# Performance work log

Hardware: AMD Instinct MI355X
Metric: run time of the kernel (lower is better)

Reference implementation:

```python
import jax, jax.numpy as jnp
import numpy as np

N, F, H = 22, 448, 64
LN_EPS = 1e-5


def _layernorm(h, g, b):
    mu = h.mean(axis=-1, keepdims=True)
    var = ((h - mu) ** 2).mean(axis=-1, keepdims=True)
    return (h - mu) / jnp.sqrt(var + LN_EPS) * g + b


def setup_inputs() -> dict:
    key = jax.random.key(0)
    ks = jax.random.split(key, 16)
    B = 128
    x = jax.random.normal(ks[0], (B, N, F), dtype=jnp.float32)
    s = lambda fan_in: 1.0 / np.sqrt(fan_in)
    # correlation-branch edge_weight_net: Linear(2F,64) -> ReLU -> Linear(64,1) -> Sigmoid
    cw1 = jax.random.uniform(ks[1], (2 * F, 64), jnp.float32, -s(2 * F), s(2 * F))
    cb1 = jax.random.uniform(ks[2], (64,), jnp.float32, -s(2 * F), s(2 * F))
    cw2 = jax.random.uniform(ks[3], (64, 1), jnp.float32, -s(64), s(64))
    cb2 = jax.random.uniform(ks[4], (1,), jnp.float32, -s(64), s(64))
    # semantic branch
    emb = jax.random.normal(ks[5], (N, H), dtype=jnp.float32) * 0.01
    D = 2 * H + 2 * F
    sw1 = jax.random.uniform(ks[6], (D, H), jnp.float32, -s(D), s(D))
    sb1 = jax.random.uniform(ks[7], (H,), jnp.float32, -s(D), s(D))
    ln_g = jnp.ones((H,), jnp.float32)
    ln_b = jnp.zeros((H,), jnp.float32)
    sw2 = jax.random.uniform(ks[8], (H, H // 2), jnp.float32, -s(H), s(H))
    sb2 = jax.random.uniform(ks[9], (H // 2,), jnp.float32, -s(H), s(H))
    sw3 = jax.random.uniform(ks[10], (H // 2, 1), jnp.float32, -s(H // 2), s(H // 2))
    sb3 = jax.random.uniform(ks[11], (1,), jnp.float32, -s(H // 2), s(H // 2))
    thr = jnp.asarray(0.3, jnp.float32)
    alpha_p = jnp.asarray(0.6, jnp.float32)
    return dict(x=x, cw1=cw1, cb1=cb1, cw2=cw2, cb2=cb2, emb=emb,
                sw1=sw1, sb1=sb1, ln_g=ln_g, ln_b=ln_b,
                sw2=sw2, sb2=sb2, sw3=sw3, sb3=sb3,
                thr=thr, alpha_p=alpha_p)


def reference(x, cw1, cb1, cw2, cb2, emb, sw1, sb1, ln_g, ln_b,
              sw2, sb2, sw3, sb3, thr, alpha_p):
    B, n, f = x.shape
    eye = jnp.eye(n, dtype=x.dtype)[None]

    # ---- Correlation graph ----
    xc = x - x.mean(axis=-1, keepdims=True)
    std = jnp.std(x, axis=-1, ddof=1, keepdims=True) + 1e-8  # torch std is unbiased
    xn = xc / std
    corr = jnp.abs(jnp.einsum('bif,bjf->bij', xn, xn) / f)
    # pairwise edge features (B,N,N,2F)
    xi = jnp.broadcast_to(x[:, :, None, :], (B, n, n, f))
    xj = jnp.broadcast_to(x[:, None, :, :], (B, n, n, f))
    ef = jnp.concatenate([xi, xj], axis=-1)
    h = jax.nn.relu(ef @ cw1 + cb1)
    w_corr = jax.nn.sigmoid((h @ cw2 + cb2)[..., 0])
    g_corr = corr * w_corr + eye

    # ---- Semantic graph ----
    ei = jnp.broadcast_to(emb[None, :, None, :], (B, n, n, H))
    ej = jnp.broadcast_to(emb[None, None, :, :], (B, n, n, H))
    sf = jnp.concatenate([ei, ej, xi, xj], axis=-1)  # (B,N,N,2H+2F)
    h1 = jax.nn.relu(_layernorm(sf @ sw1 + sb1, ln_g, ln_b))
    h2 = jax.nn.relu(h1 @ sw2 + sb2)
    w_sem = jax.nn.sigmoid((h2 @ sw3 + sb3)[..., 0])  # (B,N,N)
    # original loop fills only i<j and mirrors; diagonal stays 0
    upper = jnp.triu(w_sem, k=1)
    adj = upper + jnp.swapaxes(upper, 1, 2)
    t = jax.nn.sigmoid(thr)
    adj = jnp.where(adj > t, adj, jnp.zeros_like(adj))
    g_sem = adj + eye

    # ---- Learned fusion ----
    alpha = jax.nn.sigmoid(alpha_p)
    return alpha * g_corr + (1.0 - alpha) * g_sem
```

## Files before the change

### kernel.cpp

```cpp
#include <hip/hip_runtime.h>
#include <math.h>

namespace {
constexpr int kN = 22;
constexpr int kF = 448;
constexpr int kNP = 484;
constexpr int kXStr = 452;
constexpr int kSm1 = kN * kXStr + 2 * kN;
constexpr int kAStr = 36;
constexpr int kBStr = 68;
constexpr int kPStr = 68;
constexpr int kVStr = 68;

__device__ __forceinline__ void map_slot(int s, int& i, int& j) {
    if (s < 231) {
        int rem = s, i0 = 0;
        while (rem >= 21 - i0) { rem -= 21 - i0; ++i0; }
        i = i0; j = i0 + 1 + rem;
    } else {
        i = j = s - 231;
    }
}
}

__global__ __launch_bounds__(256) void hgc_k1(
    const float* __restrict__ x,
    const float* __restrict__ cw1, const float* __restrict__ cb1,
    const float* __restrict__ emb,
    const float* __restrict__ sw1, const float* __restrict__ sb1,
    float* __restrict__ C, float* __restrict__ g,
    int M, int Mtiles, int nGemm)
{
    __shared__ __align__(16) float sm[kSm1];
    const int tid = threadIdx.x;

    if ((int)blockIdx.x < nGemm) {
        float* As = sm;
        float* Bs = sm + 64 * kAStr;
        const int bm = blockIdx.x % Mtiles;
        const int bn = blockIdx.x / Mtiles;
        const int m0 = bm * 32;

        const float* Wsrc =
            (bn == 0) ? cw1 :
            (bn == 1) ? cw1 + 448 * 64 :
            (bn == 2) ? sw1 + 128 * 64 :
                        sw1 + 576 * 64;

        const int tm = tid & 15;
        const int tn = tid >> 4;
        float acc[2][4];
        #pragma unroll
        for (int i = 0; i < 2; ++i)
            #pragma unroll
            for (int j = 0; j < 4; ++j) acc[i][j] = 0.f;

        float4 rA[2], rB[4];

        auto preMain = [&](int k0) {
            #pragma unroll
            for (int p = 0; p < 2; ++p) {
                const int idx = tid + p * 256;
                const int row = idx >> 4, kq = idx & 15;
                int m = m0 + row; if (m >= M) m = M - 1;
                rA[p] = *(const float4*)&x[(size_t)m * kF + k0 + kq * 4];
            }
            #pragma unroll
            for (int p = 0; p < 4; ++p) {
                const int idx = tid + p * 256;
                const int k = idx >> 4, nq = idx & 15;
                rB[p] = *(const float4*)&Wsrc[(size_t)(k0 + k) * 64 + nq * 4];
            }
        };
        auto preEmb = [&]() {
            const float* W2 = sw1 + (bn == 2 ? 0 : 64) * 64;
            #pragma unroll
            for (int p = 0; p < 2; ++p) {
                const int idx = tid + p * 256;
                const int row = idx >> 4, kq = idx & 15;
                const int r = (m0 + row) % kN;
                rA[p] = *(const float4*)&emb[(size_t)r * 64 + kq * 4];
            }
            #pragma unroll
            for (int p = 0; p < 4; ++p) {
                const int idx = tid + p * 256;
                const int k = idx >> 4, nq = idx & 15;
                rB[p] = *(const float4*)&W2[(size_t)k * 64 + nq * 4];
            }
        };
        auto commit = [&]() {
            #pragma unroll
            for (int p = 0; p < 2; ++p) {
                const int idx = tid + p * 256;
                const int row = idx >> 4, kq = idx & 15;
                As[(kq * 4 + 0) * kAStr + row] = rA[p].x;
                As[(kq * 4 + 1) * kAStr + row] = rA[p].y;
                As[(kq * 4 + 2) * kAStr + row] = rA[p].z;
                As[(kq * 4 + 3) * kAStr + row] = rA[p].w;
            }
            #pragma unroll
            for (int p = 0; p < 4; ++p) {
                const int idx = tid + p * 256;
                const int k = idx >> 4, nq = idx & 15;
                *(float4*)&Bs[k * kBStr + nq * 4] = rB[p];
            }
        };
        auto compute = [&]() {
            #pragma unroll 8
            for (int k = 0; k < 64; ++k) {
                const float2 a2 = *(const float2*)&As[k * kAStr + tm * 2];
                const float4 b4 = *(const float4*)&Bs[k * kBStr + tn * 4];
                acc[0][0] = fmaf(a2.x, b4.x, acc[0][0]);
                acc[0][1] = fmaf(a2.x, b4.y, acc[0][1]);
                acc[0][2] = fmaf(a2.x, b4.z, acc[0][2]);
                acc[0][3] = fmaf(a2.x, b4.w, acc[0][3]);
                acc[1][0] = fmaf(a2.y, b4.x, acc[1][0]);
                acc[1][1] = fmaf(a2.y, b4.y, acc[1][1]);
                acc[1][2] = fmaf(a2.y, b4.z, acc[1][2]);
                acc[1][3] = fmaf(a2.y, b4.w, acc[1][3]);
            }
        };

        preMain(0);
        commit();
        __syncthreads();
        for (int c = 0; c < 7; ++c) {
            if (c < 6) preMain((c + 1) * 64);
            else if (bn >= 2) preEmb();
            compute();
            __syncthreads();
            if (c < 6 || bn >= 2) {
                commit();
                __syncthreads();
            }
        }
        if (bn >= 2) compute();

        float4 bias = {0, 0, 0, 0};
        if (bn == 0)      bias = *(const float4*)&cb1[tn * 4];
        else if (bn == 2) bias = *(const float4*)&sb1[tn * 4];
        #pragma unroll
        for (int i = 0; i < 2; ++i) {
            const int m = m0 + tm * 2 + i;
            if (m < M) {
                float4 o;
                o.x = acc[i][0] + bias.x; o.y = acc[i][1] + bias.y;
                o.z = acc[i][2] + bias.z; o.w = acc[i][3] + bias.w;
                *(float4*)&C[(size_t)m * 256 + bn * 64 + tn * 4] = o;
            }
        }
    } else {
        float* smu = sm + kN * kXStr;
        float* sis = smu + kN;
        const int cb = blockIdx.x - nGemm;
        const int b = cb >> 1;
        const int r0 = (cb & 1) * 11;

        const float4* xb4 = (const float4*)(x + (size_t)b * (kN * kF));
        for (int idx = tid; idx < kN * kF / 4; idx += 256) {
            const float4 v = xb4[idx];
            const int r = idx / 112;
            const int k = (idx - r * 112) * 4;
            float* d = sm + r * kXStr + k;
            d[0] = v.x; d[1] = v.y; d[2] = v.z; d[3] = v.w;
        }
        __syncthreads();

        {
            const int wid = tid >> 6, lane = tid & 63;
            for (int r = wid; r < kN; r += 4) {
                const float* row = sm + r * kXStr;
                float s = 0.f;
                #pragma unroll
                for (int c = 0; c < 7; ++c) s += row[c * 64 + lane];
                #pragma unroll
                for (int o = 32; o; o >>= 1) s += __shfl_xor(s, o, 64);
                const float mean = s * (1.f / 448.f);
                float ss = 0.f;
                #pragma unroll
                for (int c = 0; c < 7; ++c) { const float d = row[c * 64 + lane] - mean; ss = fmaf(d, d, ss); }
                #pragma unroll
                for (int o = 32; o; o >>= 1) ss += __shfl_xor(ss, o, 64);
                if (lane == 0) {
                    smu[r] = mean;
                    sis[r] = 1.f / (sqrtf(ss * (1.f / 447.f)) + 1e-8f);
                }
            }
        }
        __syncthreads();

        for (int p = tid; p < 11 * kN; p += 256) {
            const int pi = p / 22;
            const int i = r0 + pi, j = p - pi * 22;
            const float4* ri = (const float4*)(sm + i * kXStr);
            const float4* rj = (const float4*)(sm + j * kXStr);
            float dot = 0.f;
            for (int q = 0; q < 112; ++q) {
                const float4 a = ri[q], bq = rj[q];
                dot = fmaf(a.x, bq.x, dot); dot = fmaf(a.y, bq.y, dot);
                dot = fmaf(a.z, bq.z, dot); dot = fmaf(a.w, bq.w, dot);
            }
            const float c = (dot - 448.f * smu[i] * smu[j]) * sis[i] * sis[j] * (1.f / 448.f);
            g[(size_t)b * kNP + i * 22 + j] = fabsf(c);
        }
    }
}

__global__ __launch_bounds__(256) void hgc_k2(
    const float* __restrict__ C, const float* __restrict__ g,
    const float* __restrict__ cw2, const float* __restrict__ cb2,
    const float* __restrict__ sw2, const float* __restrict__ sb2,
    const float* __restrict__ sw3, const float* __restrict__ sb3,
    const float* __restrict__ ln_g, const float* __restrict__ ln_b,
    const float* __restrict__ thr, const float* __restrict__ alpha_p,
    float* __restrict__ out)
{
    __shared__ __align__(16) float sp[4 * kN * kPStr];
    __shared__ float sg[kNP];
    __shared__ __align__(16) float sw2s[2048];
    __shared__ float scw2[64], slng[64], slnb[64], ssw3[32], ssb2[32];
    __shared__ __align__(16) float vbuf[32 * kVStr];

    const int tid = threadIdx.x;
    const int b   = blockIdx.x >> 2;
    const int pb  = blockIdx.x & 3;

    #pragma unroll
    for (int a = 0; a < 4; ++a) {
        float* dst = sp + a * kN * kPStr;
        for (int idx = tid; idx < 352; idx += 256) {
            const int r = idx >> 4, kq = idx & 15;
            const float4 v = *(const float4*)&C[((size_t)(b * 22 + r)) * 256 + a * 64 + kq * 4];
            *(float4*)&dst[r * kPStr + kq * 4] = v;
        }
    }
    for (int idx = tid; idx < kNP; idx += 256) sg[idx] = g[(size_t)b * kNP + idx];
    {
        const float4* s4 = (const float4*)sw2;
        for (int idx = tid; idx < 512; idx += 256)
            *((float4*)(sw2s + idx * 4)) = s4[idx];
    }
    if (tid < 64)       { scw2[tid] = cw2[tid]; slng[tid] = ln_g[tid]; slnb[tid] = ln_b[tid]; }
    else if (tid < 96)  { ssw3[tid - 64] = sw3[tid - 64]; }
    else if (tid < 128) { ssb2[tid - 96] = sb2[tid - 96]; }
    __syncthreads();

    const int pl = tid >> 3;
    const int t  = tid & 7;
    const float* sa1 = sp;
    const float* sa2 = sp + kN * kPStr;
    const float* su1 = sp + 2 * kN * kPStr;
    const float* su2 = sp + 3 * kN * kPStr;

    for (int ch = 0; ch < 2; ++ch) {
        const int s_ = pb * 64 + ch * 32 + pl;
        const bool valid = s_ < 253;
        const int s = valid ? s_ : 252;
        int i, j; map_slot(s, i, j);

        float zc1 = 0.f, zc2 = 0.f;
        {
            const float* a1i = sa1 + i * kPStr + t * 8;
            const float* a2j = sa2 + j * kPStr + t * 8;
            const float* a1j = sa1 + j * kPStr + t * 8;
            const float* a2i = sa2 + i * kPStr + t * 8;
            const float4 i0 = *(const float4*)a1i, i1 = *(const float4*)(a1i + 4);
            const float4 j0 = *(const float4*)a2j, j1 = *(const float4*)(a2j + 4);
            const float4 k0 = *(const float4*)a1j, k1 = *(const float4*)(a1j + 4);
            const float4 l0 = *(const float4*)a2i, l1 = *(const float4*)(a2i + 4);
            const float4 w0 = *(const float4*)(scw2 + t * 8);
            const float4 w1 = *(const float4*)(scw2 + t * 8 + 4);
            zc1 = fmaf(fmaxf(i0.x + j0.x, 0.f), w0.x, zc1);
            zc1 = fmaf(fmaxf(i0.y + j0.y, 0.f), w0.y, zc1);
            zc1 = fmaf(fmaxf(i0.z + j0.z, 0.f), w0.z, zc1);
            zc1 = fmaf(fmaxf(i0.w + j0.w, 0.f), w0.w, zc1);
            zc1 = fmaf(fmaxf(i1.x + j1.x, 0.f), w1.x, zc1);
            zc1 = fmaf(fmaxf(i1.y + j1.y, 0.f), w1.y, zc1);
            zc1 = fmaf(fmaxf(i1.z + j1.z, 0.f), w1.z, zc1);
            zc1 = fmaf(fmaxf(i1.w + j1.w, 0.f), w1.w, zc1);
            zc2 = fmaf(fmaxf(k0.x + l0.x, 0.f), w0.x, zc2);
            zc2 = fmaf(fmaxf(k0.y + l0.y, 0.f), w0.y, zc2);
            zc2 = fmaf(fmaxf(k0.z + l0.z, 0.f), w0.z, zc2);
            zc2 = fmaf(fmaxf(k0.w + l0.w, 0.f), w0.w, zc2);
            zc2 = fmaf(fmaxf(k1.x + l1.x, 0.f), w1.x, zc2);
            zc2 = fmaf(fmaxf(k1.y + l1.y, 0.f), w1.y, zc2);
            zc2 = fmaf(fmaxf(k1.z + l1.z, 0.f), w1.z, zc2);
            zc2 = fmaf(fmaxf(k1.w + l1.w, 0.f), w1.w, zc2);
            zc1 += __shfl_xor(zc1, 1, 64); zc1 += __shfl_xor(zc1, 2, 64); zc1 += __shfl_xor(zc1, 4, 64);
            zc2 += __shfl_xor(zc2, 1, 64); zc2 += __shfl_xor(zc2, 2, 64); zc2 += __shfl_xor(zc2, 4, 64);
        }

        float raw[8];
        float s1 = 0.f;
        {
            const float* pu1 = su1 + i * kPStr + t * 8;
            const float* pu2 = su2 + j * kPStr + t * 8;
            const float4 u0 = *(const float4*)pu1, u1v = *(const float4*)(pu1 + 4);
            const float4 v0 = *(const float4*)pu2, v1v = *(const float4*)(pu2 + 4);
            raw[0] = u0.x + v0.x; raw[1] = u0.y + v0.y; raw[2] = u0.z + v0.z; raw[3] = u0.w + v0.w;
            raw[4] = u1v.x + v1v.x; raw[5] = u1v.y + v1v.y; raw[6] = u1v.z + v1v.z; raw[7] = u1v.w + v1v.w;
            #pragma unroll
            for (int c = 0; c < 8; ++c) s1 += raw[c];
        }
        s1 += __shfl_xor(s1, 1, 64); s1 += __shfl_xor(s1, 2, 64); s1 += __shfl_xor(s1, 4, 64);
        const float mean = s1 * (1.f / 64.f);
        float s2 = 0.f;
        #pragma unroll
        for (int c = 0; c < 8; ++c) { const float d = raw[c] - mean; s2 = fmaf(d, d, s2); }
        s2 += __shfl_xor(s2, 1, 64); s2 += __shfl_xor(s2, 2, 64); s2 += __shfl_xor(s2, 4, 64);
        const float rstd = rsqrtf(s2 * (1.f / 64.f) + 1e-5f);
        {
            float* vb = vbuf + pl * kVStr + t * 8;
            float4 o0, o1;
            o0.x = fmaxf(fmaf((raw[0] - mean) * rstd, slng[t*8+0], slnb[t*8+0]), 0.f);
            o0.y = fmaxf(fmaf((raw[1] - mean) * rstd, slng[t*8+1], slnb[t*8+1]), 0.f);
            o0.z = fmaxf(fmaf((raw[2] - mean) * rstd, slng[t*8+2], slnb[t*8+2]), 0.f);
            o0.w = fmaxf(fmaf((raw[3] - mean) * rstd, slng[t*8+3], slnb[t*8+3]), 0.f);
            o1.x = fmaxf(fmaf((raw[4] - mean) * rstd, slng[t*8+4], slnb[t*8+4]), 0.f);
            o1.y = fmaxf(fmaf((raw[5] - mean) * rstd, slng[t*8+5], slnb[t*8+5]), 0.f);
            o1.z = fmaxf(fmaf((raw[6] - mean) * rstd, slng[t*8+6], slnb[t*8+6]), 0.f);
            o1.w = fmaxf(fmaf((raw[7] - mean) * rstd, slng[t*8+7], slnb[t*8+7]), 0.f);
            *(float4*)vb = o0;
            *(float4*)(vb + 4) = o1;
        }
        __syncthreads();

        float4 acc = {0, 0, 0, 0};
        {
            const float* vb = vbuf + pl * kVStr;
            for (int k = 0; k < 64; ++k) {
                const float v = vb[k];
                const float4 w = *((const float4*)(sw2s + k * 32 + t * 4));
                acc.x = fmaf(v, w.x, acc.x); acc.y = fmaf(v, w.y, acc.y);
                acc.z = fmaf(v, w.z, acc.z); acc.w = fmaf(v, w.w, acc.w);
            }
        }
        float z2;
        {
            const int o0 = t * 4;
            z2  = fmaxf(acc.x + ssb2[o0 + 0], 0.f) * ssw3[o0 + 0];
            z2 += fmaxf(acc.y + ssb2[o0 + 1], 0.f) * ssw3[o0 + 1];
            z2 += fmaxf(acc.z + ssb2[o0 + 2], 0.f) * ssw3[o0 + 2];
            z2 += fmaxf(acc.w + ssb2[o0 + 3], 0.f) * ssw3[o0 + 3];
            z2 += __shfl_xor(z2, 1, 64); z2 += __shfl_xor(z2, 2, 64); z2 += __shfl_xor(z2, 4, 64);
        }

        if (valid && t == 0) {
            const float alpha = 1.f / (1.f + __expf(-alpha_p[0]));
            const float wc1 = 1.f / (1.f + __expf(-(zc1 + cb2[0])));
            float gsem;
            if (i == j) {
                gsem = 1.f;
            } else {
                const float wsem = 1.f / (1.f + expf(-(z2 + sb3[0])));
                const float tt   = 1.f / (1.f + expf(-thr[0]));
                gsem = (wsem > tt) ? wsem : 0.f;
            }
            const float gc1 = fmaf(sg[i * 22 + j], wc1, (i == j) ? 1.f : 0.f);
            out[(size_t)b * kNP + i * 22 + j] = fmaf(alpha, gc1, (1.f - alpha) * gsem);
            if (i != j) {
                const float wc2 = 1.f / (1.f + __expf(-(zc2 + cb2[0])));
                const float gc2 = sg[j * 22 + i] * wc2;
                out[(size_t)b * kNP + j * 22 + i] = fmaf(alpha, gc2, (1.f - alpha) * gsem);
            }
        }
        __syncthreads();
    }
}

extern "C" void kernel_launch(void* const* d_in, const int* in_sizes, int n_in,
                              void* d_out, int out_size, void* d_ws, size_t ws_size,
                              hipStream_t stream)
{
    (void)n_in; (void)out_size; (void)ws_size;
    const float* x     = (const float*)d_in[0];
    const float* cw1   = (const float*)d_in[1];
    const float* cb1   = (const float*)d_in[2];
    const float* cw2   = (const float*)d_in[3];
    const float* cb2   = (const float*)d_in[4];
    const float* emb   = (const float*)d_in[5];
    const float* sw1   = (const float*)d_in[6];
    const float* sb1   = (const float*)d_in[7];
    const float* ln_g  = (const float*)d_in[8];
    const float* ln_b  = (const float*)d_in[9];
    const float* sw2   = (const float*)d_in[10];
    const float* sb2   = (const float*)d_in[11];
    const float* sw3   = (const float*)d_in[12];
    const float* sb3   = (const float*)d_in[13];
    const float* thr   = (const float*)d_in[14];
    const float* alpha = (const float*)d_in[15];
    float* out = (float*)d_out;
    float* ws  = (float*)d_ws;

    const int B = in_sizes[0] / (kN * kF);
    const int M = kN * B;
    const int Mtiles = (M + 31) / 32;
    const int nGemm = Mtiles * 4;

    float* C = ws;
    float* g = ws + (size_t)M * 256;

    hipLaunchKernelGGL(hgc_k1, dim3(nGemm + 2 * B), dim3(256), 0, stream,
                       x, cw1, cb1, emb, sw1, sb1, C, g, M, Mtiles, nGemm);
    hipLaunchKernelGGL(hgc_k2, dim3(4 * B), dim3(256), 0, stream,
                       C, g, cw2, cb2, sw2, sb2, sw3, sb3, ln_g, ln_b, thr, alpha, out);
}
```

Before: 126.8 us.

## Split-K GEMM tiles with 4x4 microtiles and single-pass transposed pair MLP

The projection GEMM in kernel 1 now splits the K dimension of each 64-wide chunk across two 128-thread halves. Each thread computes a 4x4 register microtile, and the two partial sums are combined through shared memory before bias and store. Kernel 2 now handles all 64 pair slots in one pass with 4 threads per slot instead of two 32-slot chunks, writing LayerNorm outputs transposed so the second-layer matvec can reuse each weight load across two slots. This cuts synchronisation rounds and LDS traffic per FMA, at the cost of an extra reduction step and more registers.

After: 128.9 us. About the same (+1.7%).

```diff
diff --git a/kernel.cpp b/kernel.cpp
--- a/kernel.cpp
+++ b/kernel.cpp
@@ -10,7 +10,7 @@
 constexpr int kAStr = 36;
 constexpr int kBStr = 68;
 constexpr int kPStr = 68;
-constexpr int kVStr = 68;
+constexpr int kTStr = 66;
 
 __device__ __forceinline__ void map_slot(int s, int& i, int& j) {
     if (s < 231) {
@@ -47,13 +47,13 @@
             (bn == 2) ? sw1 + 128 * 64 :
                         sw1 + 576 * 64;
 
-        const int tm = tid & 15;
-        const int tn = tid >> 4;
-        float acc[2][4];
+        const int kg   = tid >> 7;
+        const int t128 = tid & 127;
+        const int mg = t128 >> 4;
+        const int ng = t128 & 15;
+        float4 acc[4];
         #pragma unroll
-        for (int i = 0; i < 2; ++i)
-            #pragma unroll
-            for (int j = 0; j < 4; ++j) acc[i][j] = 0.f;
+        for (int i = 0; i < 4; ++i) acc[i] = float4{0, 0, 0, 0};
 
         float4 rA[2], rB[4];
 
@@ -107,17 +107,18 @@
         };
         auto compute = [&]() {
             #pragma unroll 8
-            for (int k = 0; k < 64; ++k) {
-                const float2 a2 = *(const float2*)&As[k * kAStr + tm * 2];
-                const float4 b4 = *(const float4*)&Bs[k * kBStr + tn * 4];
-                acc[0][0] = fmaf(a2.x, b4.x, acc[0][0]);
-                acc[0][1] = fmaf(a2.x, b4.y, acc[0][1]);
-                acc[0][2] = fmaf(a2.x, b4.z, acc[0][2]);
-                acc[0][3] = fmaf(a2.x, b4.w, acc[0][3]);
-                acc[1][0] = fmaf(a2.y, b4.x, acc[1][0]);
-                acc[1][1] = fmaf(a2.y, b4.y, acc[1][1]);
-                acc[1][2] = fmaf(a2.y, b4.z, acc[1][2]);
-                acc[1][3] = fmaf(a2.y, b4.w, acc[1][3]);
+            for (int kk = 0; kk < 32; ++kk) {
+                const int k = kg * 32 + kk;
+                const float4 a4 = *(const float4*)&As[k * kAStr + mg * 4];
+                const float4 b4 = *(const float4*)&Bs[k * kBStr + ng * 4];
+                acc[0].x = fmaf(a4.x, b4.x, acc[0].x); acc[0].y = fmaf(a4.x, b4.y, acc[0].y);
+                acc[0].z = fmaf(a4.x, b4.z, acc[0].z); acc[0].w = fmaf(a4.x, b4.w, acc[0].w);
+                acc[1].x = fmaf(a4.y, b4.x, acc[1].x); acc[1].y = fmaf(a4.y, b4.y, acc[1].y);
+                acc[1].z = fmaf(a4.y, b4.z, acc[1].z); acc[1].w = fmaf(a4.y, b4.w, acc[1].w);
+                acc[2].x = fmaf(a4.z, b4.x, acc[2].x); acc[2].y = fmaf(a4.z, b4.y, acc[2].y);
+                acc[2].z = fmaf(a4.z, b4.z, acc[2].z); acc[2].w = fmaf(a4.z, b4.w, acc[2].w);
+                acc[3].x = fmaf(a4.w, b4.x, acc[3].x); acc[3].y = fmaf(a4.w, b4.y, acc[3].y);
+                acc[3].z = fmaf(a4.w, b4.z, acc[3].z); acc[3].w = fmaf(a4.w, b4.w, acc[3].w);
             }
         };
 
@@ -136,17 +137,28 @@
         }
         if (bn >= 2) compute();
 
-        float4 bias = {0, 0, 0, 0};
-        if (bn == 0)      bias = *(const float4*)&cb1[tn * 4];
-        else if (bn == 2) bias = *(const float4*)&sb1[tn * 4];
-        #pragma unroll
-        for (int i = 0; i < 2; ++i) {
-            const int m = m0 + tm * 2 + i;
-            if (m < M) {
-                float4 o;
-                o.x = acc[i][0] + bias.x; o.y = acc[i][1] + bias.y;
-                o.z = acc[i][2] + bias.z; o.w = acc[i][3] + bias.w;
-                *(float4*)&C[(size_t)m * 256 + bn * 64 + tn * 4] = o;
+        __syncthreads();
+        float* red = sm;
+        if (kg == 1) {
+            #pragma unroll
+            for (int i = 0; i < 4; ++i)
+                *(float4*)&red[i * 512 + t128 * 4] = acc[i];
+        }
+        __syncthreads();
+        if (kg == 0) {
+            float4 bias = {0, 0, 0, 0};
+            if (bn == 0)      bias = *(const float4*)&cb1[ng * 4];
+            else if (bn == 2) bias = *(const float4*)&sb1[ng * 4];
+            #pragma unroll
+            for (int i = 0; i < 4; ++i) {
+                const float4 r = *(const float4*)&red[i * 512 + t128 * 4];
+                const int m = m0 + mg * 4 + i;
+                if (m < M) {
+                    float4 o;
+                    o.x = acc[i].x + r.x + bias.x; o.y = acc[i].y + r.y + bias.y;
+                    o.z = acc[i].z + r.z + bias.z; o.w = acc[i].w + r.w + bias.w;
+                    *(float4*)&C[(size_t)m * 256 + bn * 64 + ng * 4] = o;
+                }
             }
         }
     } else {
@@ -219,7 +231,8 @@
     __shared__ float sg[kNP];
     __shared__ __align__(16) float sw2s[2048];
     __shared__ float scw2[64], slng[64], slnb[64], ssw3[32], ssb2[32];
-    __shared__ __align__(16) float vbuf[32 * kVStr];
+    __shared__ float szc[128];
+    __shared__ __align__(16) float vbT[64 * kTStr];
 
     const int tid = threadIdx.x;
     const int b   = blockIdx.x >> 2;
@@ -245,126 +258,130 @@
     else if (tid < 128) { ssb2[tid - 96] = sb2[tid - 96]; }
     __syncthreads();
 
-    const int pl = tid >> 3;
-    const int t  = tid & 7;
     const float* sa1 = sp;
     const float* sa2 = sp + kN * kPStr;
     const float* su1 = sp + 2 * kN * kPStr;
     const float* su2 = sp + 3 * kN * kPStr;
 
-    for (int ch = 0; ch < 2; ++ch) {
-        const int s_ = pb * 64 + ch * 32 + pl;
-        const bool valid = s_ < 253;
-        const int s = valid ? s_ : 252;
+    {
+        const int sl = tid >> 2, t4 = tid & 3;
+        const int s_ = pb * 64 + sl;
+        const int s = (s_ < 253) ? s_ : 252;
         int i, j; map_slot(s, i, j);
 
         float zc1 = 0.f, zc2 = 0.f;
         {
-            const float* a1i = sa1 + i * kPStr + t * 8;
-            const float* a2j = sa2 + j * kPStr + t * 8;
-            const float* a1j = sa1 + j * kPStr + t * 8;
-            const float* a2i = sa2 + i * kPStr + t * 8;
-            const float4 i0 = *(const float4*)a1i, i1 = *(const float4*)(a1i + 4);
-            const float4 j0 = *(const float4*)a2j, j1 = *(const float4*)(a2j + 4);
-            const float4 k0 = *(const float4*)a1j, k1 = *(const float4*)(a1j + 4);
-            const float4 l0 = *(const float4*)a2i, l1 = *(const float4*)(a2i + 4);
-            const float4 w0 = *(const float4*)(scw2 + t * 8);
-            const float4 w1 = *(const float4*)(scw2 + t * 8 + 4);
-            zc1 = fmaf(fmaxf(i0.x + j0.x, 0.f), w0.x, zc1);
-            zc1 = fmaf(fmaxf(i0.y + j0.y, 0.f), w0.y, zc1);
-            zc1 = fmaf(fmaxf(i0.z + j0.z, 0.f), w0.z, zc1);
-            zc1 = fmaf(fmaxf(i0.w + j0.w, 0.f), w0.w, zc1);
-            zc1 = fmaf(fmaxf(i1.x + j1.x, 0.f), w1.x, zc1);
-            zc1 = fmaf(fmaxf(i1.y + j1.y, 0.f), w1.y, zc1);
-            zc1 = fmaf(fmaxf(i1.z + j1.z, 0.f), w1.z, zc1);
-            zc1 = fmaf(fmaxf(i1.w + j1.w, 0.f), w1.w, zc1);
-            zc2 = fmaf(fmaxf(k0.x + l0.x, 0.f), w0.x, zc2);
-            zc2 = fmaf(fmaxf(k0.y + l0.y, 0.f), w0.y, zc2);
-            zc2 = fmaf(fmaxf(k0.z + l0.z, 0.f), w0.z, zc2);
-            zc2 = fmaf(fmaxf(k0.w + l0.w, 0.f), w0.w, zc2);
-            zc2 = fmaf(fmaxf(k1.x + l1.x, 0.f), w1.x, zc2);
-            zc2 = fmaf(fmaxf(k1.y + l1.y, 0.f), w1.y, zc2);
-            zc2 = fmaf(fmaxf(k1.z + l1.z, 0.f), w1.z, zc2);
-            zc2 = fmaf(fmaxf(k1.w + l1.w, 0.f), w1.w, zc2);
-            zc1 += __shfl_xor(zc1, 1, 64); zc1 += __shfl_xor(zc1, 2, 64); zc1 += __shfl_xor(zc1, 4, 64);
-            zc2 += __shfl_xor(zc2, 1, 64); zc2 += __shfl_xor(zc2, 2, 64); zc2 += __shfl_xor(zc2, 4, 64);
-        }
-
-        float raw[8];
+            const float* a1i = sa1 + i * kPStr + t4 * 16;
+            const float* a2j = sa2 + j * kPStr + t4 * 16;
+            const float* a1j = sa1 + j * kPStr + t4 * 16;
+            const float* a2i = sa2 + i * kPStr + t4 * 16;
+            #pragma unroll
+            for (int c4 = 0; c4 < 4; ++c4) {
+                const float4 p = *(const float4*)(a1i + c4 * 4);
+                const float4 q = *(const float4*)(a2j + c4 * 4);
+                const float4 r = *(const float4*)(a1j + c4 * 4);
+                const float4 t = *(const float4*)(a2i + c4 * 4);
+                const float4 w = *(const float4*)(scw2 + t4 * 16 + c4 * 4);
+                zc1 = fmaf(fmaxf(p.x + q.x, 0.f), w.x, zc1);
+                zc1 = fmaf(fmaxf(p.y + q.y, 0.f), w.y, zc1);
+                zc1 = fmaf(fmaxf(p.z + q.z, 0.f), w.z, zc1);
+                zc1 = fmaf(fmaxf(p.w + q.w, 0.f), w.w, zc1);
+                zc2 = fmaf(fmaxf(r.x + t.x, 0.f), w.x, zc2);
+                zc2 = fmaf(fmaxf(r.y + t.y, 0.f), w.y, zc2);
+                zc2 = fmaf(fmaxf(r.z + t.z, 0.f), w.z, zc2);
+                zc2 = fmaf(fmaxf(r.w + t.w, 0.f), w.w, zc2);
+            }
+            zc1 += __shfl_xor(zc1, 1, 64); zc1 += __shfl_xor(zc1, 2, 64);
+            zc2 += __shfl_xor(zc2, 1, 64); zc2 += __shfl_xor(zc2, 2, 64);
+            if (t4 == 0) { szc[sl * 2] = zc1; szc[sl * 2 + 1] = zc2; }
+        }
+
+        float raw[16];
         float s1 = 0.f;
         {
-            const float* pu1 = su1 + i * kPStr + t * 8;
-            const float* pu2 = su2 + j * kPStr + t * 8;
-            const float4 u0 = *(const float4*)pu1, u1v = *(const float4*)(pu1 + 4);
-            const float4 v0 = *(const float4*)pu2, v1v = *(const float4*)(pu2 + 4);
-            raw[0] = u0.x + v0.x; raw[1] = u0.y + v0.y; raw[2] = u0.z + v0.z; raw[3] = u0.w + v0.w;
-            raw[4] = u1v.x + v1v.x; raw[5] = u1v.y + v1v.y; raw[6] = u1v.z + v1v.z; raw[7] = u1v.w + v1v.w;
-            #pragma unroll
-            for (int c = 0; c < 8; ++c) s1 += raw[c];
-        }
-        s1 += __shfl_xor(s1, 1, 64); s1 += __shfl_xor(s1, 2, 64); s1 += __shfl_xor(s1, 4, 64);
+            const float* pu1 = su1 + i * kPStr + t4 * 16;
+            const float* pu2 = su2 + j * kPStr + t4 * 16;
+            #pragma unroll
+            for (int c4 = 0; c4 < 4; ++c4) {
+                const float4 a = *(const float4*)(pu1 + c4 * 4);
+                const float4 e = *(const float4*)(pu2 + c4 * 4);
+                raw[c4*4+0] = a.x + e.x; raw[c4*4+1] = a.y + e.y;
+                raw[c4*4+2] = a.z + e.z; raw[c4*4+3] = a.w + e.w;
+                s1 += raw[c4*4+0] + raw[c4*4+1] + raw[c4*4+2] + raw[c4*4+3];
+            }
+        }
+        s1 += __shfl_xor(s1, 1, 64); s1 += __shfl_xor(s1, 2, 64);
         const float mean = s1 * (1.f / 64.f);
         float s2 = 0.f;
         #pragma unroll
-        for (int c = 0; c < 8; ++c) { const float d = raw[c] - mean; s2 = fmaf(d, d, s2); }
-        s2 += __shfl_xor(s2, 1, 64); s2 += __shfl_xor(s2, 2, 64); s2 += __shfl_xor(s2, 4, 64);
+        for (int c = 0; c < 16; ++c) { const float d = raw[c] - mean; s2 = fmaf(d, d, s2); }
+        s2 += __shfl_xor(s2, 1, 64); s2 += __shfl_xor(s2, 2, 64);
         const float rstd = rsqrtf(s2 * (1.f / 64.f) + 1e-5f);
-        {
-            float* vb = vbuf + pl * kVStr + t * 8;
-            float4 o0, o1;
-            o0.x = fmaxf(fmaf((raw[0] - mean) * rstd, slng[t*8+0], slnb[t*8+0]), 0.f);
-            o0.y = fmaxf(fmaf((raw[1] - mean) * rstd, slng[t*8+1], slnb[t*8+1]), 0.f);
-            o0.z = fmaxf(fmaf((raw[2] - mean) * rstd, slng[t*8+2], slnb[t*8+2]), 0.f);
-            o0.w = fmaxf(fmaf((raw[3] - mean) * rstd, slng[t*8+3], slnb[t*8+3]), 0.f);
-            o1.x = fmaxf(fmaf((raw[4] - mean) * rstd, slng[t*8+4], slnb[t*8+4]), 0.f);
-            o1.y = fmaxf(fmaf((raw[5] - mean) * rstd, slng[t*8+5], slnb[t*8+5]), 0.f);
-            o1.z = fmaxf(fmaf((raw[6] - mean) * rstd, slng[t*8+6], slnb[t*8+6]), 0.f);
-            o1.w = fmaxf(fmaf((raw[7] - mean) * rstd, slng[t*8+7], slnb[t*8+7]), 0.f);
-            *(float4*)vb = o0;
-            *(float4*)(vb + 4) = o1;
-        }
-        __syncthreads();
-
-        float4 acc = {0, 0, 0, 0};
-        {
-            const float* vb = vbuf + pl * kVStr;
-            for (int k = 0; k < 64; ++k) {
-                const float v = vb[k];
-                const float4 w = *((const float4*)(sw2s + k * 32 + t * 4));
-                acc.x = fmaf(v, w.x, acc.x); acc.y = fmaf(v, w.y, acc.y);
-                acc.z = fmaf(v, w.z, acc.z); acc.w = fmaf(v, w.w, acc.w);
-            }
-        }
-        float z2;
-        {
-            const int o0 = t * 4;
-            z2  = fmaxf(acc.x + ssb2[o0 + 0], 0.f) * ssw3[o0 + 0];
-            z2 += fmaxf(acc.y + ssb2[o0 + 1], 0.f) * ssw3[o0 + 1];
-            z2 += fmaxf(acc.z + ssb2[o0 + 2], 0.f) * ssw3[o0 + 2];
-            z2 += fmaxf(acc.w + ssb2[o0 + 3], 0.f) * ssw3[o0 + 3];
-            z2 += __shfl_xor(z2, 1, 64); z2 += __shfl_xor(z2, 2, 64); z2 += __shfl_xor(z2, 4, 64);
-        }
-
-        if (valid && t == 0) {
+        #pragma unroll
+        for (int c = 0; c < 16; ++c) {
+            const int k = t4 * 16 + c;
+            vbT[k * kTStr + sl] = fmaxf(fmaf((raw[c] - mean) * rstd, slng[k], slnb[k]), 0.f);
+        }
+    }
+    __syncthreads();
+
+    {
+        const int w = tid >> 6, l = tid & 63;
+        const int sg8 = l >> 3, cq = l & 7;
+        const int sl0 = w * 16 + sg8 * 2;
+        float4 a0 = {0,0,0,0}, a1 = {0,0,0,0};
+        for (int k = 0; k < 64; ++k) {
+            const float4 w4 = *(const float4*)&sw2s[k * 32 + cq * 4];
+            const float2 v2 = *(const float2*)&vbT[k * kTStr + sl0];
+            a0.x = fmaf(v2.x, w4.x, a0.x); a0.y = fmaf(v2.x, w4.y, a0.y);
+            a0.z = fmaf(v2.x, w4.z, a0.z); a0.w = fmaf(v2.x, w4.w, a0.w);
+            a1.x = fmaf(v2.y, w4.x, a1.x); a1.y = fmaf(v2.y, w4.y, a1.y);
+            a1.z = fmaf(v2.y, w4.z, a1.z); a1.w = fmaf(v2.y, w4.w, a1.w);
+        }
+        const int o0 = cq * 4;
+        float z0, z1;
+        z0  = fmaxf(a0.x + ssb2[o0+0], 0.f) * ssw3[o0+0];
+        z0 += fmaxf(a0.y + ssb2[o0+1], 0.f) * ssw3[o0+1];
+        z0 += fmaxf(a0.z + ssb2[o0+2], 0.f) * ssw3[o0+2];
+        z0 += fmaxf(a0.w + ssb2[o0+3], 0.f) * ssw3[o0+3];
+        z1  = fmaxf(a1.x + ssb2[o0+0], 0.f) * ssw3[o0+0];
+        z1 += fmaxf(a1.y + ssb2[o0+1], 0.f) * ssw3[o0+1];
+        z1 += fmaxf(a1.z + ssb2[o0+2], 0.f) * ssw3[o0+2];
+        z1 += fmaxf(a1.w + ssb2[o0+3], 0.f) * ssw3[o0+3];
+        z0 += __shfl_xor(z0, 1, 64); z0 += __shfl_xor(z0, 2, 64); z0 += __shfl_xor(z0, 4, 64);
+        z1 += __shfl_xor(z1, 1, 64); z1 += __shfl_xor(z1, 2, 64); z1 += __shfl_xor(z1, 4, 64);
+
+        if (cq == 0) {
             const float alpha = 1.f / (1.f + __expf(-alpha_p[0]));
-            const float wc1 = 1.f / (1.f + __expf(-(zc1 + cb2[0])));
-            float gsem;
-            if (i == j) {
-                gsem = 1.f;
-            } else {
-                const float wsem = 1.f / (1.f + expf(-(z2 + sb3[0])));
-                const float tt   = 1.f / (1.f + expf(-thr[0]));
-                gsem = (wsem > tt) ? wsem : 0.f;
-            }
-            const float gc1 = fmaf(sg[i * 22 + j], wc1, (i == j) ? 1.f : 0.f);
-            out[(size_t)b * kNP + i * 22 + j] = fmaf(alpha, gc1, (1.f - alpha) * gsem);
-            if (i != j) {
-                const float wc2 = 1.f / (1.f + __expf(-(zc2 + cb2[0])));
-                const float gc2 = sg[j * 22 + i] * wc2;
-                out[(size_t)b * kNP + j * 22 + i] = fmaf(alpha, gc2, (1.f - alpha) * gsem);
-            }
-        }
-        __syncthreads();
+            const float cb2s  = cb2[0];
+            #pragma unroll
+            for (int e = 0; e < 2; ++e) {
+                const int sl = sl0 + e;
+                const float z = e ? z1 : z0;
+                const int s_ = pb * 64 + sl;
+                if (s_ < 253) {
+                    int i, j; map_slot(s_, i, j);
+                    const float zc1 = szc[sl * 2];
+                    const float zc2 = szc[sl * 2 + 1];
+                    const float wc1 = 1.f / (1.f + __expf(-(zc1 + cb2s)));
+                    float gsem;
+                    if (i == j) {
+                        gsem = 1.f;
+                    } else {
+                        const float wsem = 1.f / (1.f + expf(-(z + sb3[0])));
+                        const float tt   = 1.f / (1.f + expf(-thr[0]));
+                        gsem = (wsem > tt) ? wsem : 0.f;
+                    }
+                    const float gc1 = fmaf(sg[i * 22 + j], wc1, (i == j) ? 1.f : 0.f);
+                    out[(size_t)b * kNP + i * 22 + j] = fmaf(alpha, gc1, (1.f - alpha) * gsem);
+                    if (i != j) {
+                        const float wc2 = 1.f / (1.f + __expf(-(zc2 + cb2s)));
+                        const float gc2 = sg[j * 22 + i] * wc2;
+                        out[(size_t)b * kNP + j * 22 + i] = fmaf(alpha, gc2, (1.f - alpha) * gsem);
+                    }
+                }
+            }
+        }
     }
 }
 
```
